# Kernel optimization log

Measured on AMD Instinct MI355X. Metric: run time of the kernel, lower is better.

Reference implementation:

```python
import jax, jax.numpy as jnp
import numpy as np

N_DET = 32

def _nuc_features(nuc_coords, nuc_charges, nuc_mask):
    # masked mean-centering of nuclear coords, then concat charge feature
    m = nuc_mask[:, None].astype(nuc_coords.dtype)  # [n_nuc, 1]
    mean = (nuc_coords * m).sum(0, keepdims=True) / jnp.maximum(m.sum(0, keepdims=True), 1.0)
    centered = nuc_coords - mean
    feats = jnp.concatenate([nuc_charges[:, None], centered], axis=-1)  # [n_nuc, 4]
    return feats * m

def _spin_orbitals(e_coords, e_mask, nuc_coords, feats, nuc_mask, W_pi, W_zeta):
    # exponent factors / nuclear weights via per-nucleus linear maps, then transpose
    zeta = (feats @ W_pi).T   # exponent_factors [n_det*max_e, n_nuc]
    pi = (feats @ W_zeta).T   # nuclear_weights  [n_det*max_e, n_nuc]
    # masked pairwise electron-nucleus distances
    diff = e_coords[:, None, :] - nuc_coords[None, :, :]          # [n_e, n_nuc, 3]
    dist_mask = e_mask[:, None] & nuc_mask[None, :]               # [n_e, n_nuc]
    d2 = (diff * diff).sum(-1)
    dist = jnp.sqrt(jnp.where(dist_mask, d2, 1.0))                # safe sqrt on masked entries
    # exp-decay envelope, masked, weighted sum over nuclei
    expo = jnp.where(dist_mask[:, None, :],
                     jnp.exp(-jnp.abs(dist[:, None, :] * zeta[None])), 0.0)  # [n_e, nd*me, n_nuc]
    orb = (pi[None] * expo).sum(-1)                               # [n_e, nd*me]
    n_e = e_coords.shape[0]
    orb = orb.reshape(n_e, N_DET, -1).swapaxes(-2, -3)            # [n_det, n_e, max_e]
    sm = e_mask[:, None] & e_mask[None, :]
    return jnp.where(sm, orb, jnp.eye(n_e, dtype=orb.dtype))


def setup_inputs() -> dict:
    key = jax.random.key(0)
    ks = jax.random.split(key, 8)
    ME, MN = 128, 128
    f = jnp.float32
    return {
        "up_coords": jax.random.normal(ks[0], (ME, 3), f),
        "down_coords": jax.random.normal(ks[1], (ME, 3), f),
        "nuc_coords": jax.random.normal(ks[2], (MN, 3), f),
        "nuc_charges": jax.random.uniform(ks[3], (MN,), f),
        "W_pi_up": jax.random.normal(ks[4], (4, N_DET * ME), f),
        "W_zeta_up": jax.random.normal(ks[5], (4, N_DET * ME), f),
        "W_pi_down": jax.random.normal(ks[6], (4, N_DET * ME), f),
        "W_zeta_down": jax.random.normal(ks[7], (4, N_DET * ME), f),
        "up_mask": jnp.ones((ME,), bool),
        "down_mask": jnp.ones((ME,), bool),
        "nuc_mask": jnp.ones((MN,), bool),
    }


def reference(up_coords, down_coords, nuc_coords, nuc_charges,
              W_pi_up, W_zeta_up, W_pi_down, W_zeta_down,
              up_mask, down_mask, nuc_mask):
    feats = _nuc_features(nuc_coords, nuc_charges, nuc_mask)
    up = _spin_orbitals(up_coords, up_mask, nuc_coords, feats, nuc_mask, W_pi_up, W_zeta_up)
    down = _spin_orbitals(down_coords, down_mask, nuc_coords, feats, nuc_mask, W_pi_down, W_zeta_down)
    return jnp.stack([up, down])  # [2, n_det, n_e, max_e]
```

## Files before the change

### kernel.cpp

```cpp
#include <hip/hip_runtime.h>
#include <cstddef>

#define NDET 32
#define ME   128
#define MN   128
#define EBLK 8
#define NOUT (NDET * ME)
#define LOG2E 1.4426950408889634f

#if __has_builtin(__builtin_amdgcn_exp2f)
#define EXP2(x) __builtin_amdgcn_exp2f(x)
#else
#define EXP2(x) exp2f(x)
#endif

typedef float v2f __attribute__((ext_vector_type(2)));

__global__ __launch_bounds__(512, 8) void env_kernel(
    const float* __restrict__ up_coords,
    const float* __restrict__ down_coords,
    const float* __restrict__ nuc_coords,
    const float* __restrict__ nuc_charges,
    const float* __restrict__ W_pi_up,
    const float* __restrict__ W_zeta_up,
    const float* __restrict__ W_pi_down,
    const float* __restrict__ W_zeta_down,
    float* __restrict__ out)
{
    __shared__ float4 feats4[MN];
    __shared__ float  duv[MN * EBLK];
    __shared__ float  ecl[EBLK * 3];
    __shared__ float  msum[2][3];
    __shared__ float4 red[3][128][2];

    const int tid = (int)threadIdx.x;
    const int e0  = (int)blockIdx.x * EBLK;
    const int d   = (int)blockIdx.y;
    const int s   = (int)blockIdx.z;

    const float* ec = s ? down_coords : up_coords;
    const float* We = s ? W_pi_down   : W_pi_up;
    const float* Ww = s ? W_zeta_down : W_zeta_up;

    if (tid < MN) {
        feats4[tid] = make_float4(nuc_charges[tid],
                                  nuc_coords[tid * 3 + 0],
                                  nuc_coords[tid * 3 + 1],
                                  nuc_coords[tid * 3 + 2]);
    } else if (tid < MN + EBLK * 3) {
        ecl[tid - MN] = ec[e0 * 3 + (tid - MN)];
    }
    __syncthreads();

    if (tid < MN) {
        float4 f = feats4[tid];
        float sx = f.y, sy = f.z, sz = f.w;
        #pragma unroll
        for (int off = 32; off > 0; off >>= 1) {
            sx += __shfl_xor(sx, off);
            sy += __shfl_xor(sy, off);
            sz += __shfl_xor(sz, off);
        }
        if ((tid & 63) == 0) {
            const int w = tid >> 6;
            msum[w][0] = sx; msum[w][1] = sy; msum[w][2] = sz;
        }
    }
    __syncthreads();

    const float mx = (msum[0][0] + msum[1][0]) * (1.f / MN);
    const float my = (msum[0][1] + msum[1][1]) * (1.f / MN);
    const float mz = (msum[0][2] + msum[1][2]) * (1.f / MN);

    {
        const int n = tid >> 2;
        const int q = tid & 3;
        const float4 f = feats4[n];
        float r[2];
        #pragma unroll
        for (int i = 0; i < 2; ++i) {
            const int e = q * 2 + i;
            const float dx = ecl[e * 3 + 0] - f.y;
            const float dy = ecl[e * 3 + 1] - f.z;
            const float dz = ecl[e * 3 + 2] - f.w;
            r[i] = sqrtf(fmaf(dx, dx, fmaf(dy, dy, dz * dz))) * (-LOG2E);
        }
        *(float2*)&duv[n * EBLK + q * 2] = make_float2(r[0], r[1]);
    }
    __syncthreads();

    if (tid < MN) {
        float4 f = feats4[tid];
        feats4[tid] = make_float4(f.x, f.y - mx, f.z - my, f.w - mz);
    }
    __syncthreads();

    const int j = tid & 127;
    const int g = tid >> 7;
    const int o = d * ME + j;

    const v2f w0 = { We[0*NOUT+o], Ww[0*NOUT+o] };
    const v2f w1 = { We[1*NOUT+o], Ww[1*NOUT+o] };
    const v2f w2 = { We[2*NOUT+o], Ww[2*NOUT+o] };
    const v2f w3 = { We[3*NOUT+o], Ww[3*NOUT+o] };

    v2f acc01 = {0.f, 0.f}, acc23 = {0.f, 0.f}, acc45 = {0.f, 0.f}, acc67 = {0.f, 0.f};

    const float4* du4 = (const float4*)duv;
    const int nbeg = g * 32;
    #pragma unroll 8
    for (int n = nbeg; n < nbeg + 32; ++n) {
        const float4 f = feats4[n];
        v2f zp = f.x * w0 + (f.y * w1 + (f.z * w2 + f.w * w3));
        const float az = __builtin_fabsf(zp.x);
        const v2f az2 = {az, az};
        const v2f pi2 = {zp.y, zp.y};
        const float4 u0 = du4[n * 2 + 0];
        const float4 u1 = du4[n * 2 + 1];
        v2f t01 = (v2f){u0.x, u0.y} * az2;
        v2f t23 = (v2f){u0.z, u0.w} * az2;
        v2f t45 = (v2f){u1.x, u1.y} * az2;
        v2f t67 = (v2f){u1.z, u1.w} * az2;
        t01.x = EXP2(t01.x); t01.y = EXP2(t01.y);
        t23.x = EXP2(t23.x); t23.y = EXP2(t23.y);
        t45.x = EXP2(t45.x); t45.y = EXP2(t45.y);
        t67.x = EXP2(t67.x); t67.y = EXP2(t67.y);
        acc01 = acc01 + pi2 * t01;
        acc23 = acc23 + pi2 * t23;
        acc45 = acc45 + pi2 * t45;
        acc67 = acc67 + pi2 * t67;
    }

    if (g) {
        red[g - 1][j][0] = make_float4(acc01.x, acc01.y, acc23.x, acc23.y);
        red[g - 1][j][1] = make_float4(acc45.x, acc45.y, acc67.x, acc67.y);
    }
    __syncthreads();
    if (!g) {
        float4 p0 = red[0][j][0], p1 = red[0][j][1];
        const float4 q0 = red[1][j][0], q1 = red[1][j][1];
        const float4 r0 = red[2][j][0], r1 = red[2][j][1];
        p0.x += q0.x + r0.x; p0.y += q0.y + r0.y;
        p0.z += q0.z + r0.z; p0.w += q0.w + r0.w;
        p1.x += q1.x + r1.x; p1.y += q1.y + r1.y;
        p1.z += q1.z + r1.z; p1.w += q1.w + r1.w;
        float* op = out + ((((size_t)s * NDET + d) * ME + e0) * ME + j);
        op[0 * ME] = acc01.x + p0.x;
        op[1 * ME] = acc01.y + p0.y;
        op[2 * ME] = acc23.x + p0.z;
        op[3 * ME] = acc23.y + p0.w;
        op[4 * ME] = acc45.x + p1.x;
        op[5 * ME] = acc45.y + p1.y;
        op[6 * ME] = acc67.x + p1.z;
        op[7 * ME] = acc67.y + p1.w;
    }
}

extern "C" void kernel_launch(void* const* d_in, const int* in_sizes, int n_in,
                              void* d_out, int out_size, void* d_ws, size_t ws_size,
                              hipStream_t stream)
{
    (void)in_sizes; (void)n_in; (void)out_size; (void)d_ws; (void)ws_size;
    env_kernel<<<dim3(ME / EBLK, NDET, 2), 512, 0, stream>>>(
        (const float*)d_in[0],
        (const float*)d_in[1],
        (const float*)d_in[2],
        (const float*)d_in[3],
        (const float*)d_in[4],
        (const float*)d_in[5],
        (const float*)d_in[6],
        (const float*)d_in[7],
        (float*)d_out);
}
```

Baseline: 89.78 us.

## Fold mean-centering into weights and broadcast distances via readlane

The per-nucleus mean subtraction is folded into a per-thread constant (negC) computed from the weights, which removes the feats4 rewrite pass and two barriers. Each wave now loads its 32 nuclei's distance values into registers once, and the inner loop broadcasts them with scalar readlane instead of reading them from shared memory every iteration. The accumulation is rewritten as scalar FMAs. A barrier is added before the reduction writes. Readlane with a compile-time lane index depends on full unrolling, and the scalar-to-vector moves and extra register pressure could cost throughput.

```diff
diff --git a/kernel.cpp b/kernel.cpp
--- a/kernel.cpp
+++ b/kernel.cpp
@@ -16,6 +16,10 @@
 
 typedef float v2f __attribute__((ext_vector_type(2)));
 
+__device__ __forceinline__ float rdlane(float v, int lane) {
+    return __uint_as_float(__builtin_amdgcn_readlane(__float_as_uint(v), lane));
+}
+
 __global__ __launch_bounds__(512, 8) void env_kernel(
     const float* __restrict__ up_coords,
     const float* __restrict__ down_coords,
@@ -28,7 +32,7 @@
     float* __restrict__ out)
 {
     __shared__ float4 feats4[MN];
-    __shared__ float  duv[MN * EBLK];
+    __shared__ __align__(16) float duv[MN * EBLK];
     __shared__ float  ecl[EBLK * 3];
     __shared__ float  msum[2][3];
     __shared__ float4 red[3][128][2];
@@ -66,11 +70,6 @@
             msum[w][0] = sx; msum[w][1] = sy; msum[w][2] = sz;
         }
     }
-    __syncthreads();
-
-    const float mx = (msum[0][0] + msum[1][0]) * (1.f / MN);
-    const float my = (msum[0][1] + msum[1][1]) * (1.f / MN);
-    const float mz = (msum[0][2] + msum[1][2]) * (1.f / MN);
 
     {
         const int n = tid >> 2;
@@ -89,51 +88,45 @@
     }
     __syncthreads();
 
-    if (tid < MN) {
-        float4 f = feats4[tid];
-        feats4[tid] = make_float4(f.x, f.y - mx, f.z - my, f.w - mz);
-    }
-    __syncthreads();
+    const float mx = (msum[0][0] + msum[1][0]) * (1.f / MN);
+    const float my = (msum[0][1] + msum[1][1]) * (1.f / MN);
+    const float mz = (msum[0][2] + msum[1][2]) * (1.f / MN);
 
     const int j = tid & 127;
     const int g = tid >> 7;
     const int o = d * ME + j;
+    const int nbeg = g * 32;
 
     const v2f w0 = { We[0*NOUT+o], Ww[0*NOUT+o] };
     const v2f w1 = { We[1*NOUT+o], Ww[1*NOUT+o] };
     const v2f w2 = { We[2*NOUT+o], Ww[2*NOUT+o] };
     const v2f w3 = { We[3*NOUT+o], Ww[3*NOUT+o] };
+    const v2f negC = -(mx * w1 + (my * w2 + mz * w3));
 
-    v2f acc01 = {0.f, 0.f}, acc23 = {0.f, 0.f}, acc45 = {0.f, 0.f}, acc67 = {0.f, 0.f};
+    const int lane = tid & 63;
+    const float4 dq = *(const float4*)&duv[(nbeg + (lane & 31)) * EBLK + (lane >> 5) * 4];
+    const float dr[4] = { dq.x, dq.y, dq.z, dq.w };
 
-    const float4* du4 = (const float4*)duv;
-    const int nbeg = g * 32;
-    #pragma unroll 8
-    for (int n = nbeg; n < nbeg + 32; ++n) {
-        const float4 f = feats4[n];
-        v2f zp = f.x * w0 + (f.y * w1 + (f.z * w2 + f.w * w3));
+    float acc[EBLK] = {0.f, 0.f, 0.f, 0.f, 0.f, 0.f, 0.f, 0.f};
+
+    #pragma unroll
+    for (int nl = 0; nl < 32; ++nl) {
+        const float4 f = feats4[nbeg + nl];
+        v2f zp = f.x * w0 + (f.y * w1 + (f.z * w2 + (f.w * w3 + negC)));
         const float az = __builtin_fabsf(zp.x);
-        const v2f az2 = {az, az};
-        const v2f pi2 = {zp.y, zp.y};
-        const float4 u0 = du4[n * 2 + 0];
-        const float4 u1 = du4[n * 2 + 1];
-        v2f t01 = (v2f){u0.x, u0.y} * az2;
-        v2f t23 = (v2f){u0.z, u0.w} * az2;
-        v2f t45 = (v2f){u1.x, u1.y} * az2;
-        v2f t67 = (v2f){u1.z, u1.w} * az2;
-        t01.x = EXP2(t01.x); t01.y = EXP2(t01.y);
-        t23.x = EXP2(t23.x); t23.y = EXP2(t23.y);
-        t45.x = EXP2(t45.x); t45.y = EXP2(t45.y);
-        t67.x = EXP2(t67.x); t67.y = EXP2(t67.y);
-        acc01 = acc01 + pi2 * t01;
-        acc23 = acc23 + pi2 * t23;
-        acc45 = acc45 + pi2 * t45;
-        acc67 = acc67 + pi2 * t67;
+        const float pi = zp.y;
+        #pragma unroll
+        for (int e = 0; e < EBLK; ++e) {
+            const float du = rdlane(dr[e & 3], (e >> 2) * 32 + nl);
+            const float t  = EXP2(du * az);
+            acc[e] = fmaf(pi, t, acc[e]);
+        }
     }
 
+    __syncthreads();
     if (g) {
-        red[g - 1][j][0] = make_float4(acc01.x, acc01.y, acc23.x, acc23.y);
-        red[g - 1][j][1] = make_float4(acc45.x, acc45.y, acc67.x, acc67.y);
+        red[g - 1][j][0] = make_float4(acc[0], acc[1], acc[2], acc[3]);
+        red[g - 1][j][1] = make_float4(acc[4], acc[5], acc[6], acc[7]);
     }
     __syncthreads();
     if (!g) {
@@ -145,14 +138,14 @@
         p1.x += q1.x + r1.x; p1.y += q1.y + r1.y;
         p1.z += q1.z + r1.z; p1.w += q1.w + r1.w;
         float* op = out + ((((size_t)s * NDET + d) * ME + e0) * ME + j);
-        op[0 * ME] = acc01.x + p0.x;
-        op[1 * ME] = acc01.y + p0.y;
-        op[2 * ME] = acc23.x + p0.z;
-        op[3 * ME] = acc23.y + p0.w;
-        op[4 * ME] = acc45.x + p1.x;
-        op[5 * ME] = acc45.y + p1.y;
-        op[6 * ME] = acc67.x + p1.z;
-        op[7 * ME] = acc67.y + p1.w;
+        op[0 * ME] = acc[0] + p0.x;
+        op[1 * ME] = acc[1] + p0.y;
+        op[2 * ME] = acc[2] + p0.z;
+        op[3 * ME] = acc[3] + p0.w;
+        op[4 * ME] = acc[4] + p1.x;
+        op[5 * ME] = acc[5] + p1.y;
+        op[6 * ME] = acc[6] + p1.z;
+        op[7 * ME] = acc[7] + p1.w;
     }
 }
 
```

Result: slower. 95.49 us (+6.4%).
